# Optimization experiments

Hardware: AMD Instinct MI355X
Metric: run time of the kernel (lower is better)

Reference implementation:

```python
import jax, jax.numpy as jnp
import numpy as np

B, S, E, H = 2, 2048, 2048, 32
D = E // H
SCALE = D ** -0.5
LN_EPS = 1e-5
NEG = -1e9  # finite large-negative for masked logits (avoids NaN grads)


def setup_inputs() -> dict:
    key = jax.random.key(0)
    ks = jax.random.split(key, 12)
    hidden_states = jax.random.normal(ks[0], (B, S, E), dtype=jnp.float32)
    # additive causal mask, shape (B, 1, S, S) as the module requires
    causal = jnp.where(jnp.tril(jnp.ones((S, S), dtype=bool)), 0.0, NEG).astype(jnp.float32)
    attention_mask = jnp.broadcast_to(causal[None, None], (B, 1, S, S))
    p = lambda k: jax.random.normal(k, (E, E), dtype=jnp.float32) * 0.02
    Wq, Wk, Wv, Wo = p(ks[1]), p(ks[2]), p(ks[3]), p(ks[4])
    bq = jax.random.normal(ks[5], (E,), dtype=jnp.float32) * 0.02
    bk = jax.random.normal(ks[6], (E,), dtype=jnp.float32) * 0.02
    bv = jax.random.normal(ks[7], (E,), dtype=jnp.float32) * 0.02
    bo = jax.random.normal(ks[8], (E,), dtype=jnp.float32) * 0.02
    ln_gamma = jnp.ones((E,), dtype=jnp.float32)
    ln_beta = jnp.zeros((E,), dtype=jnp.float32)
    return {"hidden_states": hidden_states, "attention_mask": attention_mask,
            "Wq": Wq, "bq": bq, "Wk": Wk, "bk": bk, "Wv": Wv, "bv": bv,
            "Wo": Wo, "bo": bo, "ln_gamma": ln_gamma, "ln_beta": ln_beta}


def _shape(x):  # [B,S,E] -> [B,H,S,D]
    return x.reshape(B, S, H, D).transpose(0, 2, 1, 3)


def reference(hidden_states, attention_mask, Wq, bq, Wk, bk, Wv, bv, Wo, bo, ln_gamma, ln_beta):
    q = _shape((hidden_states @ Wq.T + bq) * SCALE)   # [B,H,S,D]
    k = _shape(hidden_states @ Wk.T + bk)
    v = _shape(hidden_states @ Wv.T + bv)
    attn_weights = jnp.einsum('bhsd,bhtd->bhst', q, k) + attention_mask
    attn_weights = jax.nn.softmax(attn_weights, axis=-1)
    ctx = jnp.einsum('bhst,bhtd->bhsd', attn_weights, v)  # [B,H,S,D]
    ctx = ctx.transpose(0, 2, 1, 3).reshape(B, S, E)
    # inner attention LayerNorm
    mu = jnp.mean(ctx, axis=-1, keepdims=True)
    var = jnp.var(ctx, axis=-1, keepdims=True)
    ctx = (ctx - mu) * jax.lax.rsqrt(var + LN_EPS) * ln_gamma + ln_beta
    return ctx @ Wo.T + bo
```

## Files before the change

### kernel.cpp

```cpp
#include <hip/hip_runtime.h>
#include <hip/hip_bf16.h>
#include <cstdint>
#include <cstddef>

#define BB 2
#define SEQ 2048
#define EMB 2048
#define NH 32
#define HD 64
#define QSCALE2 0.18033688011112042f

#if __has_builtin(__builtin_amdgcn_exp2f)
#define EXP2(x) __builtin_amdgcn_exp2f(x)
#else
#define EXP2(x) exp2f(x)
#endif

typedef __hip_bfloat16 bf16;
typedef __attribute__((ext_vector_type(8))) short short8;
typedef __attribute__((ext_vector_type(4))) float floatx4;

__device__ __forceinline__ floatx4 mfma16(short8 a, short8 b, floatx4 c) {
    return __builtin_amdgcn_mfma_f32_16x16x32_bf16(a, b, c, 0, 0, 0);
}

__device__ __forceinline__ void gl_lds16(const void* g, void* s) {
    __builtin_amdgcn_global_load_lds((const __attribute__((address_space(1))) void*)g,
                                     (__attribute__((address_space(3))) void*)s,
                                     16, 0, 0);
}

__device__ __forceinline__ unsigned bfbits(float x) {
    union { bf16 h; unsigned short u; } c;
    c.h = __float2bfloat16(x);
    return (unsigned)c.u;
}

#define NX4 2097152
#define NW4 1048576
__global__ __launch_bounds__(256) void f2ball(
    const float4* __restrict__ X,  const float4* __restrict__ Wq,
    const float4* __restrict__ Wk, const float4* __restrict__ Wv,
    const float4* __restrict__ Wo, uint2* __restrict__ dst,
    const float* __restrict__ gamma, const float* __restrict__ beta,
    float* __restrict__ uv)
{
    const int tid = threadIdx.x;
    int i = blockIdx.x * 256 + tid;
    const bool isWo = (i >= NX4 + 3 * NW4);

    if (!isWo) {
        const float4* src;
        int si;
        if (i < NX4) { src = X; si = i; }
        else {
            int j = i - NX4;
            int w = j >> 20;
            si = j & (NW4 - 1);
            src = (w == 0) ? Wq : (w == 1) ? Wk : Wv;
        }
        float4 v4 = src[si];
        union { bf16 h[4]; uint2 u; } p;
        p.h[0] = __float2bfloat16(v4.x);
        p.h[1] = __float2bfloat16(v4.y);
        p.h[2] = __float2bfloat16(v4.z);
        p.h[3] = __float2bfloat16(v4.w);
        dst[i] = p.u;
        return;
    }

    int j = i - (NX4 + 3 * NW4);
    int n = j >> 9;
    int k4 = (j & 511) * 4;
    float4 w  = Wo[j];
    float4 g  = *(const float4*)&gamma[k4];
    float4 be = *(const float4*)&beta[k4];
    float4 wg = make_float4(w.x * g.x, w.y * g.y, w.z * g.z, w.w * g.w);
    union { bf16 h[4]; uint2 u; } p;
    p.h[0] = __float2bfloat16(wg.x);
    p.h[1] = __float2bfloat16(wg.y);
    p.h[2] = __float2bfloat16(wg.z);
    p.h[3] = __float2bfloat16(wg.w);
    dst[i] = p.u;

    float su = wg.x + wg.y + wg.z + wg.w;
    float sv = w.x * be.x + w.y * be.y + w.z * be.z + w.w * be.w;
#pragma unroll
    for (int off = 1; off < 64; off <<= 1) {
        su += __shfl_xor(su, off);
        sv += __shfl_xor(sv, off);
    }
    __shared__ float red[2][4];
    int wid = tid >> 6, lane = tid & 63;
    if (lane == 0) { red[0][wid] = su; red[1][wid] = sv; }
    __syncthreads();
    if (tid == 0) {
        atomicAdd(&uv[n],        red[0][0] + red[0][1] + red[0][2] + red[0][3]);
        atomicAdd(&uv[2048 + n], red[1][0] + red[1][1] + red[1][2] + red[1][3]);
    }
}

#define GSTAGE(SRC, R0, KSTR, DST)                                        \
    _Pragma("unroll")                                                     \
    for (int i_ = 0; i_ < 4; ++i_) {                                      \
        int l_ = tid + i_ * 256;                                          \
        int r_ = l_ >> 3;                                                 \
        int g_ = ((l_ & 7) ^ (r_ & 7)) << 3;                              \
        gl_lds16(SRC + (size_t)((R0) + r_) * (KSTR) + kb + g_, &DST[l_ * 8]); \
    }

__device__ __forceinline__ short8 frag64(const bf16* S, int row, int grp, int sw) {
    return *(const short8*)&S[row * 64 + ((grp ^ sw) << 3)];
}

__global__ __launch_bounds__(256, 2) void gemm_qkv(
    const bf16* __restrict__ Xb, const bf16* __restrict__ Wqk,
    const bf16* __restrict__ Wv,
    const float* __restrict__ bq, const float* __restrict__ bk,
    const float* __restrict__ bv,
    bf16* __restrict__ Qo, bf16* __restrict__ Ko, bf16* __restrict__ Vt)
{
    __shared__ bf16 As[128 * 64];
    __shared__ bf16 Bs[128 * 64];

    const int bx = blockIdx.x, by = blockIdx.y;
    const bool isV = (bx >= 32);
    const bf16* Ap; const bf16* Wp; int row0, col0;
    if (!isV) { Ap = Xb; row0 = by * 128;        Wp = Wqk; col0 = bx * 128; }
    else      { Ap = Wv; row0 = (bx - 32) * 128; Wp = Xb;  col0 = by * 128; }

    const int tid  = threadIdx.x;
    const int wid  = tid >> 6;
    const int lane = tid & 63;
    const int quad = lane >> 4;
    const int l16  = lane & 15;
    const int sw   = l16 & 7;
    const int wr   = wid >> 1;
    const int wc   = wid & 1;

    floatx4 acc[4][4] = {};

    for (int kb = 0; kb < EMB; kb += 64) {
        GSTAGE(Ap, row0, EMB, As);
        GSTAGE(Wp, col0, EMB, Bs);
        __syncthreads();

        short8 af[4][2], bfm[4][2];
#pragma unroll
        for (int i = 0; i < 4; ++i) {
            int row = wr * 64 + i * 16 + l16;
            af[i][0] = frag64(As, row, quad, sw);
            af[i][1] = frag64(As, row, quad + 4, sw);
        }
#pragma unroll
        for (int j = 0; j < 4; ++j) {
            int row = wc * 64 + j * 16 + l16;
            bfm[j][0] = frag64(Bs, row, quad, sw);
            bfm[j][1] = frag64(Bs, row, quad + 4, sw);
        }
#pragma unroll
        for (int kh = 0; kh < 2; ++kh)
#pragma unroll
            for (int i = 0; i < 4; ++i)
#pragma unroll
                for (int j = 0; j < 4; ++j)
                    acc[i][j] = mfma16(af[i][kh], bfm[j][kh], acc[i][j]);
        __syncthreads();
    }

    if (!isV) {
        const bool isQ = (bx < 16);
        bf16* base = isQ ? Qo : Ko;
        const float* bias = isQ ? bq : bk;
        const float sc = isQ ? QSCALE2 : 1.f;
        const int cb = isQ ? col0 : col0 - EMB;
#pragma unroll
        for (int i = 0; i < 4; ++i) {
            int row = row0 + wr * 64 + i * 16 + quad * 4;
#pragma unroll
            for (int j = 0; j < 4; ++j) {
                int col = cb + wc * 64 + j * 16 + l16;
                float b = bias[col];
#pragma unroll
                for (int r = 0; r < 4; ++r)
                    base[(size_t)(row + r) * EMB + col] =
                        __float2bfloat16((acc[i][j][r] + b) * sc);
            }
        }
    } else {
#pragma unroll
        for (int i = 0; i < 4; ++i) {
            int frow = row0 + wr * 64 + i * 16 + quad * 4;
#pragma unroll
            for (int j = 0; j < 4; ++j) {
                int tok = col0 + wc * 64 + j * 16 + l16;
#pragma unroll
                for (int r = 0; r < 4; ++r)
                    Vt[(size_t)(frow + r) * (BB * SEQ) + tok] =
                        __float2bfloat16(acc[i][j][r] + bv[frow + r]);
            }
        }
    }
}

__global__ __launch_bounds__(256, 2) void gemm_out(
    const bf16* __restrict__ A, const bf16* __restrict__ W,
    const float* __restrict__ bias, const float* __restrict__ ssum,
    const float* __restrict__ ssq, const float* __restrict__ uv,
    float* __restrict__ C)
{
    __shared__ bf16 As[128 * 64];
    __shared__ bf16 Bs[128 * 64];

    const int tid  = threadIdx.x;
    const int wid  = tid >> 6;
    const int lane = tid & 63;
    const int quad = lane >> 4;
    const int l16  = lane & 15;
    const int sw   = l16 & 7;
    const int wr   = wid >> 1;
    const int wc   = wid & 1;
    const int row0 = blockIdx.y * 128;
    const int col0 = blockIdx.x * 128;

    floatx4 acc[4][4] = {};

    for (int kb = 0; kb < EMB; kb += 64) {
        GSTAGE(A, row0, EMB, As);
        GSTAGE(W, col0, EMB, Bs);
        __syncthreads();

        short8 af[4][2], bfm[4][2];
#pragma unroll
        for (int i = 0; i < 4; ++i) {
            int row = wr * 64 + i * 16 + l16;
            af[i][0] = frag64(As, row, quad, sw);
            af[i][1] = frag64(As, row, quad + 4, sw);
        }
#pragma unroll
        for (int j = 0; j < 4; ++j) {
            int row = wc * 64 + j * 16 + l16;
            bfm[j][0] = frag64(Bs, row, quad, sw);
            bfm[j][1] = frag64(Bs, row, quad + 4, sw);
        }
#pragma unroll
        for (int kh = 0; kh < 2; ++kh)
#pragma unroll
            for (int i = 0; i < 4; ++i)
#pragma unroll
                for (int j = 0; j < 4; ++j)
                    acc[i][j] = mfma16(af[i][kh], bfm[j][kh], acc[i][j]);
        __syncthreads();
    }

#pragma unroll
    for (int i = 0; i < 4; ++i) {
        int row = row0 + wr * 64 + i * 16 + quad * 4;
#pragma unroll
        for (int r = 0; r < 4; ++r) {
            float mu  = ssum[row + r] * (1.f / EMB);
            float var = ssq[row + r] * (1.f / EMB) - mu * mu;
            float rs  = rsqrtf(var + 1e-5f);
            float rmu = rs * mu;
#pragma unroll
            for (int j = 0; j < 4; ++j) {
                int col = col0 + wc * 64 + j * 16 + l16;
                C[(size_t)(row + r) * EMB + col] =
                    rs * acc[i][j][r] - rmu * uv[col] + uv[2048 + col] + bias[col];
            }
        }
    }
}

__global__ __launch_bounds__(256, 3) void attn(
    const bf16* __restrict__ Q, const bf16* __restrict__ K,
    const bf16* __restrict__ Vt, bf16* __restrict__ ctx,
    float* __restrict__ ssum, float* __restrict__ ssq)
{
    const int bh   = blockIdx.x;
    const int pair = blockIdx.y;
    const int b    = bh >> 5;
    const int h    = bh & 31;
    const int tid  = threadIdx.x;
    const int wid  = tid >> 6;
    const int lane = tid & 63;
    const int quad = lane >> 4;
    const int l16  = lane & 15;
    const int sw8  = l16 & 7;
    const int NT   = SEQ / 128;

    __shared__ bf16 Ks[2][64 * 64];
    __shared__ bf16 Vts[2][64 * 64];
    __shared__ bf16 Ps[4][32 * 72];

    const size_t bhoff = (size_t)b * SEQ * EMB + (size_t)h * HD;
    const size_t vtoff = (size_t)(h * HD) * (BB * SEQ) + (size_t)b * SEQ;

    short8 ones;
#pragma unroll
    for (int i = 0; i < 8; ++i) ones[i] = (short)0x3F80;

#define STAGE(kc, bufi)                                                         \
    {                                                                           \
        _Pragma("unroll")                                                       \
        for (int i = 0; i < 2; ++i) {                                           \
            int l = tid + i * 256;                                              \
            int r8 = l >> 3;                                                    \
            int g = (((l & 7) ^ (r8 & 7)) << 3);                                \
            gl_lds16(K + bhoff + (size_t)((kc) * 64 + r8) * EMB + g,            \
                     &Ks[bufi][l * 8]);                                         \
        }                                                                       \
        _Pragma("unroll")                                                       \
        for (int i = 0; i < 2; ++i) {                                           \
            int l = tid + i * 256;                                              \
            int r8 = l >> 3;                                                    \
            int g = (((l & 7) ^ (r8 & 7)) << 3);                                \
            gl_lds16(Vt + vtoff + (size_t)r8 * (BB * SEQ) + (kc) * 64 + g,      \
                     &Vts[bufi][l * 8]);                                        \
        }                                                                       \
    }

    for (int t = 0; t < 2; ++t) {
        const int qt = t ? pair : (NT - 1 - pair);
        const int qbase = qt * 128;

        short8 qf[2][2];
#pragma unroll
        for (int mi = 0; mi < 2; ++mi) {
            int qrow = qbase + wid * 32 + mi * 16 + l16;
            const bf16* qp = Q + bhoff + (size_t)qrow * EMB + quad * 8;
            qf[mi][0] = *(const short8*)qp;
            qf[mi][1] = *(const short8*)(qp + 32);
        }

        floatx4 o[2][4] = {};
        floatx4 ol[2] = {};
        int tb[2];
        tb[0] = (qbase + wid * 32) >> 6;
        tb[1] = (qbase + wid * 32 + 16) >> 6;
        const int nchunks = 2 * qt + 2;

        __syncthreads();
        STAGE(0, 0);

        for (int kc = 0; kc < nchunks; ++kc) {
            const int buf = kc & 1;
            __syncthreads();
            if (kc + 1 < nchunks) STAGE(kc + 1, buf ^ 1);

            floatx4 st[4][2];
#pragma unroll
            for (int kt = 0; kt < 4; ++kt) {
                int row = kt * 16 + l16;
                short8 kf0 = *(const short8*)&Ks[buf][row * 64 + ((quad ^ sw8) << 3)];
                short8 kf1 = *(const short8*)&Ks[buf][row * 64 + (((quad + 4) ^ sw8) << 3)];
#pragma unroll
                for (int mi = 0; mi < 2; ++mi) {
                    floatx4 z = {};
                    st[kt][mi] = mfma16(kf1, qf[mi][1], mfma16(kf0, qf[mi][0], z));
                }
            }

#pragma unroll
            for (int mi = 0; mi < 2; ++mi) {
                int qrow = qbase + wid * 32 + mi * 16 + l16;
                if (kc >= tb[mi]) {
#pragma unroll
                    for (int kt = 0; kt < 4; ++kt) {
                        int keyb = kc * 64 + kt * 16 + quad * 4;
#pragma unroll
                        for (int r = 0; r < 4; ++r)
                            if (keyb + r > qrow) st[kt][mi][r] = -1e9f;
                    }
                }
#pragma unroll
                for (int kt = 0; kt < 4; ++kt) {
                    unsigned lo = bfbits(EXP2(st[kt][mi][0])) |
                                  (bfbits(EXP2(st[kt][mi][1])) << 16);
                    unsigned hi = bfbits(EXP2(st[kt][mi][2])) |
                                  (bfbits(EXP2(st[kt][mi][3])) << 16);
                    *(uint2*)&Ps[wid][(mi * 16 + l16) * 72 + kt * 16 + quad * 4] =
                        make_uint2(lo, hi);
                }
            }

            short8 pf[2][2];
#pragma unroll
            for (int mi = 0; mi < 2; ++mi) {
                pf[mi][0] = *(const short8*)&Ps[wid][(mi * 16 + l16) * 72 + quad * 8];
                pf[mi][1] = *(const short8*)&Ps[wid][(mi * 16 + l16) * 72 + 32 + quad * 8];
            }
#pragma unroll
            for (int n = 0; n < 4; ++n) {
                int row = n * 16 + l16;
                short8 vf0 = *(const short8*)&Vts[buf][row * 64 + ((quad ^ sw8) << 3)];
                short8 vf1 = *(const short8*)&Vts[buf][row * 64 + (((quad + 4) ^ sw8) << 3)];
#pragma unroll
                for (int mi = 0; mi < 2; ++mi)
                    o[mi][n] = mfma16(pf[mi][1], vf1, mfma16(pf[mi][0], vf0, o[mi][n]));
            }
#pragma unroll
            for (int mi = 0; mi < 2; ++mi)
                ol[mi] = mfma16(pf[mi][1], ones, mfma16(pf[mi][0], ones, ol[mi]));
        }

#pragma unroll
        for (int mi = 0; mi < 2; ++mi)
#pragma unroll
            for (int r = 0; r < 4; ++r) {
                int grow = qbase + wid * 32 + mi * 16 + quad * 4 + r;
                float inv = 1.f / ol[mi][r];
                float ps = 0.f, psq = 0.f;
#pragma unroll
                for (int n = 0; n < 4; ++n) {
                    float v = o[mi][n][r] * inv;
                    ps += v; psq += v * v;
                    ctx[bhoff + (size_t)grow * EMB + n * 16 + l16] =
                        __float2bfloat16(v);
                }
#pragma unroll
                for (int off = 1; off < 16; off <<= 1) {
                    ps  += __shfl_xor(ps, off);
                    psq += __shfl_xor(psq, off);
                }
                if (l16 == 0) {
                    atomicAdd(&ssum[b * SEQ + grow], ps);
                    atomicAdd(&ssq[b * SEQ + grow], psq);
                }
            }
    }
#undef STAGE
}

extern "C" void kernel_launch(void* const* d_in, const int* in_sizes, int n_in,
                              void* d_out, int out_size, void* d_ws, size_t ws_size,
                              hipStream_t stream) {
    const float* X     = (const float*)d_in[0];
    const float* Wq    = (const float*)d_in[2];
    const float* bq    = (const float*)d_in[3];
    const float* Wk    = (const float*)d_in[4];
    const float* bk    = (const float*)d_in[5];
    const float* Wv    = (const float*)d_in[6];
    const float* bv    = (const float*)d_in[7];
    const float* Wo    = (const float*)d_in[8];
    const float* bo    = (const float*)d_in[9];
    const float* gamma = (const float*)d_in[10];
    const float* beta  = (const float*)d_in[11];
    float* out = (float*)d_out;

    const size_t M  = (size_t)BB * SEQ;
    const size_t ME = M * EMB;
    const size_t EE = (size_t)EMB * EMB;

    const size_t need = (ME + 4 * EE + ME + ME) * sizeof(bf16) + 12288 * sizeof(float);
    if (ws_size < need) return;

    bf16* Xb   = (bf16*)d_ws;
    bf16* Wqb  = Xb  + ME;
    bf16* Wkb  = Wqb + EE;
    bf16* Wvb  = Wkb + EE;
    bf16* Wob  = Wvb + EE;
    bf16* Vt   = Wob + EE;
    bf16* ctx  = Vt  + ME;
    float* stats = (float*)(ctx + ME);
    float* ssum  = stats;
    float* ssq   = stats + M;
    float* uvv   = stats + 2 * M;
    (void)Wkb;
    bf16* Qb   = (bf16*)d_out;
    bf16* Kb   = Qb + ME;

    hipMemsetAsync(stats, 0, 12288 * sizeof(float), stream);

    dim3 blk(256);
    f2ball<<<dim3((NX4 + 4 * NW4) / 256), blk, 0, stream>>>(
        (const float4*)X, (const float4*)Wq, (const float4*)Wk,
        (const float4*)Wv, (const float4*)Wo, (uint2*)d_ws, gamma, beta, uvv);

    gemm_qkv<<<dim3(48, 32), blk, 0, stream>>>(Xb, Wqb, Wvb, bq, bk, bv, Qb, Kb, Vt);
    attn<<<dim3(BB * NH, SEQ / 256), blk, 0, stream>>>(Qb, Kb, Vt, ctx, ssum, ssq);
    gemm_out<<<dim3(EMB / 128, M / 128), blk, 0, stream>>>(
        ctx, Wob, bo, ssum, ssq, uvv, out);
}
```

Baseline: 378.5 us.

## Split attention into one q-tile per block and vectorize conversion kernel

The attention kernel now launches one block per 128-row query tile, with heavier tiles scheduled first, instead of pairing a light and a heavy tile in each block. This doubles the grid to improve load balance and occupancy. The fp32-to-bf16 conversion kernel now processes 8 elements per thread with 16-byte stores. It writes the Wo row reductions directly instead of using atomics. It also zeroes the stats buffer itself, so the separate memset launch is removed.

```diff
diff --git a/kernel.cpp b/kernel.cpp
--- a/kernel.cpp
+++ b/kernel.cpp
@@ -36,55 +36,62 @@
     return (unsigned)c.u;
 }
 
+__device__ __forceinline__ uint2 pack4(float a, float b, float c, float d) {
+    return make_uint2(bfbits(a) | (bfbits(b) << 16), bfbits(c) | (bfbits(d) << 16));
+}
+
 #define NX4 2097152
 #define NW4 1048576
+#define NBULK 10240
 __global__ __launch_bounds__(256) void f2ball(
     const float4* __restrict__ X,  const float4* __restrict__ Wq,
     const float4* __restrict__ Wk, const float4* __restrict__ Wv,
     const float4* __restrict__ Wo, uint2* __restrict__ dst,
     const float* __restrict__ gamma, const float* __restrict__ beta,
-    float* __restrict__ uv)
+    float* __restrict__ uv, float* __restrict__ stats)
 {
+    const int bx = blockIdx.x;
     const int tid = threadIdx.x;
-    int i = blockIdx.x * 256 + tid;
-    const bool isWo = (i >= NX4 + 3 * NW4);
-
-    if (!isWo) {
-        const float4* src;
-        int si;
-        if (i < NX4) { src = X; si = i; }
+
+    if (bx < NBULK) {
+        size_t g = (size_t)bx * 512 + tid * 2;
+        float4 a, b;
+        if (g < NX4) { a = X[g]; b = X[g + 1]; }
         else {
-            int j = i - NX4;
-            int w = j >> 20;
-            si = j & (NW4 - 1);
-            src = (w == 0) ? Wq : (w == 1) ? Wk : Wv;
-        }
-        float4 v4 = src[si];
-        union { bf16 h[4]; uint2 u; } p;
-        p.h[0] = __float2bfloat16(v4.x);
-        p.h[1] = __float2bfloat16(v4.y);
-        p.h[2] = __float2bfloat16(v4.z);
-        p.h[3] = __float2bfloat16(v4.w);
-        dst[i] = p.u;
+            size_t j = g - NX4;
+            int w = (int)(j >> 20);
+            size_t o = j & (NW4 - 1);
+            const float4* W = (w == 0) ? Wq : (w == 1) ? Wk : Wv;
+            a = W[o]; b = W[o + 1];
+        }
+        uint4 p;
+        uint2 lo = pack4(a.x, a.y, a.z, a.w);
+        uint2 hi = pack4(b.x, b.y, b.z, b.w);
+        p.x = lo.x; p.y = lo.y; p.z = hi.x; p.w = hi.y;
+        ((uint4*)dst)[g >> 1] = p;
+        if (bx < 8)
+            ((uint4*)stats)[bx * 256 + tid] = make_uint4(0, 0, 0, 0);
         return;
     }
 
-    int j = i - (NX4 + 3 * NW4);
-    int n = j >> 9;
-    int k4 = (j & 511) * 4;
-    float4 w  = Wo[j];
-    float4 g  = *(const float4*)&gamma[k4];
-    float4 be = *(const float4*)&beta[k4];
-    float4 wg = make_float4(w.x * g.x, w.y * g.y, w.z * g.z, w.w * g.w);
-    union { bf16 h[4]; uint2 u; } p;
-    p.h[0] = __float2bfloat16(wg.x);
-    p.h[1] = __float2bfloat16(wg.y);
-    p.h[2] = __float2bfloat16(wg.z);
-    p.h[3] = __float2bfloat16(wg.w);
-    dst[i] = p.u;
-
-    float su = wg.x + wg.y + wg.z + wg.w;
-    float sv = w.x * be.x + w.y * be.y + w.z * be.z + w.w * be.w;
+    int n = bx - NBULK;
+    size_t j0 = (size_t)n * 512 + tid * 2;
+    float4 w0 = Wo[j0], w1 = Wo[j0 + 1];
+    float4 g0 = *(const float4*)&gamma[tid * 8];
+    float4 g1 = *(const float4*)&gamma[tid * 8 + 4];
+    float4 b0 = *(const float4*)&beta[tid * 8];
+    float4 b1 = *(const float4*)&beta[tid * 8 + 4];
+    float4 wg0 = make_float4(w0.x * g0.x, w0.y * g0.y, w0.z * g0.z, w0.w * g0.w);
+    float4 wg1 = make_float4(w1.x * g1.x, w1.y * g1.y, w1.z * g1.z, w1.w * g1.w);
+    uint4 p;
+    uint2 lo = pack4(wg0.x, wg0.y, wg0.z, wg0.w);
+    uint2 hi = pack4(wg1.x, wg1.y, wg1.z, wg1.w);
+    p.x = lo.x; p.y = lo.y; p.z = hi.x; p.w = hi.y;
+    ((uint4*)dst)[((size_t)(NX4 + 3 * NW4) + j0) >> 1] = p;
+
+    float su = wg0.x + wg0.y + wg0.z + wg0.w + wg1.x + wg1.y + wg1.z + wg1.w;
+    float sv = w0.x * b0.x + w0.y * b0.y + w0.z * b0.z + w0.w * b0.w
+             + w1.x * b1.x + w1.y * b1.y + w1.z * b1.z + w1.w * b1.w;
 #pragma unroll
     for (int off = 1; off < 64; off <<= 1) {
         su += __shfl_xor(su, off);
@@ -95,8 +102,8 @@
     if (lane == 0) { red[0][wid] = su; red[1][wid] = sv; }
     __syncthreads();
     if (tid == 0) {
-        atomicAdd(&uv[n],        red[0][0] + red[0][1] + red[0][2] + red[0][3]);
-        atomicAdd(&uv[2048 + n], red[1][0] + red[1][1] + red[1][2] + red[1][3]);
+        uv[n]        = red[0][0] + red[0][1] + red[0][2] + red[0][3];
+        uv[2048 + n] = red[1][0] + red[1][1] + red[1][2] + red[1][3];
     }
 }
 
@@ -278,7 +285,7 @@
     float* __restrict__ ssum, float* __restrict__ ssq)
 {
     const int bh   = blockIdx.x;
-    const int pair = blockIdx.y;
+    const int qt   = (int)gridDim.y - 1 - blockIdx.y;
     const int b    = bh >> 5;
     const int h    = bh & 31;
     const int tid  = threadIdx.x;
@@ -287,7 +294,6 @@
     const int quad = lane >> 4;
     const int l16  = lane & 15;
     const int sw8  = l16 & 7;
-    const int NT   = SEQ / 128;
 
     __shared__ bf16 Ks[2][64 * 64];
     __shared__ bf16 Vts[2][64 * 64];
@@ -320,115 +326,108 @@
         }                                                                       \
     }
 
-    for (int t = 0; t < 2; ++t) {
-        const int qt = t ? pair : (NT - 1 - pair);
-        const int qbase = qt * 128;
-
-        short8 qf[2][2];
+    const int qbase = qt * 128;
+
+    short8 qf[2][2];
+#pragma unroll
+    for (int mi = 0; mi < 2; ++mi) {
+        int qrow = qbase + wid * 32 + mi * 16 + l16;
+        const bf16* qp = Q + bhoff + (size_t)qrow * EMB + quad * 8;
+        qf[mi][0] = *(const short8*)qp;
+        qf[mi][1] = *(const short8*)(qp + 32);
+    }
+
+    floatx4 o[2][4] = {};
+    floatx4 ol[2] = {};
+    int tb[2];
+    tb[0] = (qbase + wid * 32) >> 6;
+    tb[1] = (qbase + wid * 32 + 16) >> 6;
+    const int nchunks = 2 * qt + 2;
+
+    STAGE(0, 0);
+
+    for (int kc = 0; kc < nchunks; ++kc) {
+        const int buf = kc & 1;
+        __syncthreads();
+        if (kc + 1 < nchunks) STAGE(kc + 1, buf ^ 1);
+
+        floatx4 st[4][2];
+#pragma unroll
+        for (int kt = 0; kt < 4; ++kt) {
+            int row = kt * 16 + l16;
+            short8 kf0 = *(const short8*)&Ks[buf][row * 64 + ((quad ^ sw8) << 3)];
+            short8 kf1 = *(const short8*)&Ks[buf][row * 64 + (((quad + 4) ^ sw8) << 3)];
+#pragma unroll
+            for (int mi = 0; mi < 2; ++mi) {
+                floatx4 z = {};
+                st[kt][mi] = mfma16(kf1, qf[mi][1], mfma16(kf0, qf[mi][0], z));
+            }
+        }
+
 #pragma unroll
         for (int mi = 0; mi < 2; ++mi) {
             int qrow = qbase + wid * 32 + mi * 16 + l16;
-            const bf16* qp = Q + bhoff + (size_t)qrow * EMB + quad * 8;
-            qf[mi][0] = *(const short8*)qp;
-            qf[mi][1] = *(const short8*)(qp + 32);
-        }
-
-        floatx4 o[2][4] = {};
-        floatx4 ol[2] = {};
-        int tb[2];
-        tb[0] = (qbase + wid * 32) >> 6;
-        tb[1] = (qbase + wid * 32 + 16) >> 6;
-        const int nchunks = 2 * qt + 2;
-
-        __syncthreads();
-        STAGE(0, 0);
-
-        for (int kc = 0; kc < nchunks; ++kc) {
-            const int buf = kc & 1;
-            __syncthreads();
-            if (kc + 1 < nchunks) STAGE(kc + 1, buf ^ 1);
-
-            floatx4 st[4][2];
+            if (kc >= tb[mi]) {
+#pragma unroll
+                for (int kt = 0; kt < 4; ++kt) {
+                    int keyb = kc * 64 + kt * 16 + quad * 4;
+#pragma unroll
+                    for (int r = 0; r < 4; ++r)
+                        if (keyb + r > qrow) st[kt][mi][r] = -1e9f;
+                }
+            }
 #pragma unroll
             for (int kt = 0; kt < 4; ++kt) {
-                int row = kt * 16 + l16;
-                short8 kf0 = *(const short8*)&Ks[buf][row * 64 + ((quad ^ sw8) << 3)];
-                short8 kf1 = *(const short8*)&Ks[buf][row * 64 + (((quad + 4) ^ sw8) << 3)];
-#pragma unroll
-                for (int mi = 0; mi < 2; ++mi) {
-                    floatx4 z = {};
-                    st[kt][mi] = mfma16(kf1, qf[mi][1], mfma16(kf0, qf[mi][0], z));
-                }
-            }
-
-#pragma unroll
-            for (int mi = 0; mi < 2; ++mi) {
-                int qrow = qbase + wid * 32 + mi * 16 + l16;
-                if (kc >= tb[mi]) {
-#pragma unroll
-                    for (int kt = 0; kt < 4; ++kt) {
-                        int keyb = kc * 64 + kt * 16 + quad * 4;
-#pragma unroll
-                        for (int r = 0; r < 4; ++r)
-                            if (keyb + r > qrow) st[kt][mi][r] = -1e9f;
-                    }
-                }
-#pragma unroll
-                for (int kt = 0; kt < 4; ++kt) {
-                    unsigned lo = bfbits(EXP2(st[kt][mi][0])) |
-                                  (bfbits(EXP2(st[kt][mi][1])) << 16);
-                    unsigned hi = bfbits(EXP2(st[kt][mi][2])) |
-                                  (bfbits(EXP2(st[kt][mi][3])) << 16);
-                    *(uint2*)&Ps[wid][(mi * 16 + l16) * 72 + kt * 16 + quad * 4] =
-                        make_uint2(lo, hi);
-                }
-            }
-
-            short8 pf[2][2];
-#pragma unroll
-            for (int mi = 0; mi < 2; ++mi) {
-                pf[mi][0] = *(const short8*)&Ps[wid][(mi * 16 + l16) * 72 + quad * 8];
-                pf[mi][1] = *(const short8*)&Ps[wid][(mi * 16 + l16) * 72 + 32 + quad * 8];
-            }
+                *(uint2*)&Ps[wid][(mi * 16 + l16) * 72 + kt * 16 + quad * 4] =
+                    pack4(EXP2(st[kt][mi][0]), EXP2(st[kt][mi][1]),
+                          EXP2(st[kt][mi][2]), EXP2(st[kt][mi][3]));
+            }
+        }
+
+        short8 pf[2][2];
+#pragma unroll
+        for (int mi = 0; mi < 2; ++mi) {
+            pf[mi][0] = *(const short8*)&Ps[wid][(mi * 16 + l16) * 72 + quad * 8];
+            pf[mi][1] = *(const short8*)&Ps[wid][(mi * 16 + l16) * 72 + 32 + quad * 8];
+        }
+#pragma unroll
+        for (int n = 0; n < 4; ++n) {
+            int row = n * 16 + l16;
+            short8 vf0 = *(const short8*)&Vts[buf][row * 64 + ((quad ^ sw8) << 3)];
+            short8 vf1 = *(const short8*)&Vts[buf][row * 64 + (((quad + 4) ^ sw8) << 3)];
+#pragma unroll
+            for (int mi = 0; mi < 2; ++mi)
+                o[mi][n] = mfma16(pf[mi][1], vf1, mfma16(pf[mi][0], vf0, o[mi][n]));
+        }
+#pragma unroll
+        for (int mi = 0; mi < 2; ++mi)
+            ol[mi] = mfma16(pf[mi][1], ones, mfma16(pf[mi][0], ones, ol[mi]));
+    }
+
+#pragma unroll
+    for (int mi = 0; mi < 2; ++mi)
+#pragma unroll
+        for (int r = 0; r < 4; ++r) {
+            int grow = qbase + wid * 32 + mi * 16 + quad * 4 + r;
+            float inv = 1.f / ol[mi][r];
+            float ps = 0.f, psq = 0.f;
 #pragma unroll
             for (int n = 0; n < 4; ++n) {
-                int row = n * 16 + l16;
-                short8 vf0 = *(const short8*)&Vts[buf][row * 64 + ((quad ^ sw8) << 3)];
-                short8 vf1 = *(const short8*)&Vts[buf][row * 64 + (((quad + 4) ^ sw8) << 3)];
-#pragma unroll
-                for (int mi = 0; mi < 2; ++mi)
-                    o[mi][n] = mfma16(pf[mi][1], vf1, mfma16(pf[mi][0], vf0, o[mi][n]));
-            }
-#pragma unroll
-            for (int mi = 0; mi < 2; ++mi)
-                ol[mi] = mfma16(pf[mi][1], ones, mfma16(pf[mi][0], ones, ol[mi]));
-        }
-
-#pragma unroll
-        for (int mi = 0; mi < 2; ++mi)
-#pragma unroll
-            for (int r = 0; r < 4; ++r) {
-                int grow = qbase + wid * 32 + mi * 16 + quad * 4 + r;
-                float inv = 1.f / ol[mi][r];
-                float ps = 0.f, psq = 0.f;
-#pragma unroll
-                for (int n = 0; n < 4; ++n) {
-                    float v = o[mi][n][r] * inv;
-                    ps += v; psq += v * v;
-                    ctx[bhoff + (size_t)grow * EMB + n * 16 + l16] =
-                        __float2bfloat16(v);
-                }
-#pragma unroll
-                for (int off = 1; off < 16; off <<= 1) {
-                    ps  += __shfl_xor(ps, off);
-                    psq += __shfl_xor(psq, off);
-                }
-                if (l16 == 0) {
-                    atomicAdd(&ssum[b * SEQ + grow], ps);
-                    atomicAdd(&ssq[b * SEQ + grow], psq);
-                }
-            }
-    }
+                float v = o[mi][n][r] * inv;
+                ps += v; psq += v * v;
+                ctx[bhoff + (size_t)grow * EMB + n * 16 + l16] =
+                    __float2bfloat16(v);
+            }
+#pragma unroll
+            for (int off = 1; off < 16; off <<= 1) {
+                ps  += __shfl_xor(ps, off);
+                psq += __shfl_xor(psq, off);
+            }
+            if (l16 == 0) {
+                atomicAdd(&ssum[b * SEQ + grow], ps);
+                atomicAdd(&ssq[b * SEQ + grow], psq);
+            }
+        }
 #undef STAGE
 }
 
@@ -470,15 +469,14 @@
     bf16* Qb   = (bf16*)d_out;
     bf16* Kb   = Qb + ME;
 
-    hipMemsetAsync(stats, 0, 12288 * sizeof(float), stream);
-
     dim3 blk(256);
-    f2ball<<<dim3((NX4 + 4 * NW4) / 256), blk, 0, stream>>>(
+    f2ball<<<dim3(NBULK + 2048), blk, 0, stream>>>(
         (const float4*)X, (const float4*)Wq, (const float4*)Wk,
-        (const float4*)Wv, (const float4*)Wo, (uint2*)d_ws, gamma, beta, uvv);
+        (const float4*)Wv, (const float4*)Wo, (uint2*)d_ws, gamma, beta,
+        uvv, stats);
 
     gemm_qkv<<<dim3(48, 32), blk, 0, stream>>>(Xb, Wqb, Wvb, bq, bk, bv, Qb, Kb, Vt);
-    attn<<<dim3(BB * NH, SEQ / 256), blk, 0, stream>>>(Qb, Kb, Vt, ctx, ssum, ssq);
+    attn<<<dim3(BB * NH, SEQ / 128), blk, 0, stream>>>(Qb, Kb, Vt, ctx, ssum, ssq);
     gemm_out<<<dim3(EMB / 128, M / 128), blk, 0, stream>>>(
         ctx, Wob, bo, ssum, ssq, uvv, out);
 }
```

Measured after the change: 358.6 us. 1.06x faster.
